# Performance work log

Hardware: AMD Instinct MI355X
Metric: run time of the kernel (lower is better)

## Reference

```python
import jax, jax.numpy as jnp
import numpy as np

B, S, I, H, C = 512, 128, 64, 256, 10


def setup_inputs() -> dict:
    key = jax.random.key(0)
    ks = jax.random.split(key, 9)
    u = lambda k, shape, lo, hi: jax.random.uniform(k, shape, jnp.float32, lo, hi)
    return {
        "x": jax.random.normal(ks[0], (B, S, I), jnp.float32),
        # LTCCell params (uniform init per init_parameters)
        "W_gd": u(ks[1], (2 * H, I + H), -0.1, 0.1),
        "b_gd": u(ks[2], (2 * H,), -0.1, 0.1),
        "W_tau": u(ks[3], (H, H), -0.1, 0.1),
        "b_tau": u(ks[4], (H,), -0.1, 0.1),
        "gleak": u(ks[5], (H,), 0.001, 1.0),
        "cm": u(ks[6], (H,), 0.4, 0.6),
        # classifier head
        "W_fc": jax.random.normal(ks[7], (C, H), jnp.float32) * 0.05,
        "b_fc": jax.random.normal(ks[8], (C,), jnp.float32) * 0.05,
    }


def reference(x, W_gd, b_gd, W_tau, b_tau, gleak, cm, W_fc, b_fc):
    # Constant part of the denominator (elementwise, hidden_dim)
    const_den = jax.nn.softplus(cm) + jax.nn.softplus(gleak)  # [H]

    def dhdt(h, x_t):
        # LTCCell.forward: dh/dt
        combined = jnp.concatenate([x_t, h], axis=1)          # [B, I+H]
        gd = combined @ W_gd.T + b_gd                          # [B, 2H]
        gate, dyn = jnp.split(gd, 2, axis=1)
        tau = jax.nn.softplus(h @ W_tau.T + b_tau)             # [B, H]
        num = jax.nn.sigmoid(gate) * jnp.tanh(dyn) - h
        return num / (tau + const_den + 1e-6)

    def step(h, x_t):
        # torchdiffeq 'rk4' fixed-grid = 3/8-rule RK4, single step dt=1 over [0,1]
        k1 = dhdt(h, x_t)
        k2 = dhdt(h + k1 / 3.0, x_t)
        k3 = dhdt(h + (k2 - k1 / 3.0), x_t)
        k4 = dhdt(h + (k1 - k2 + k3), x_t)
        h_new = h + (k1 + 3.0 * (k2 + k3) + k4) * 0.125
        return h_new, None

    h0 = jnp.zeros((x.shape[0], H), x.dtype)
    xs = jnp.transpose(x, (1, 0, 2))                           # [S, B, I]
    h_final, _ = jax.lax.scan(step, h0, xs)
    return h_final @ W_fc.T + b_fc                             # [B, C]
```

## Files before the change

### kernel.cpp

```cpp
#include <hip/hip_runtime.h>

typedef __attribute__((ext_vector_type(8))) short bf16x8;
typedef __attribute__((ext_vector_type(4))) float f32x4;
typedef __attribute__((ext_vector_type(2))) _Float16 f16x2;

#define MFMA(a, b, c) __builtin_amdgcn_mfma_f32_16x16x32_bf16((a), (b), (c), 0, 0, 0)

__device__ __forceinline__ unsigned short f2bf(float f) {
    unsigned int u = __builtin_bit_cast(unsigned int, f);
    return (unsigned short)((u + 0x7FFFu + ((u >> 16) & 1u)) >> 16);
}
__device__ __forceinline__ float softplusf(float v) {
    return __logf(1.f + __expf(v));
}

__global__ __launch_bounds__(256) void prepack_kernel(const float* __restrict__ W_gd,
                                                      unsigned short* __restrict__ ws) {
    int i = blockIdx.x * 256 + threadIdx.x;
    ws[i] = f2bf(W_gd[(256 + (i >> 8)) * 320 + 64 + (i & 255)]);
    if (i < 32768) ws[65536 + i] = f2bf(W_gd[(i >> 6) * 320 + (i & 63)]);
}

__global__ __launch_bounds__(512, 1)
void ltc_kernel(
    const float* __restrict__ x, const float* __restrict__ W_gd,
    const float* __restrict__ b_gd, const float* __restrict__ W_tau,
    const float* __restrict__ b_tau, const float* __restrict__ gleak,
    const float* __restrict__ cm, const float* __restrict__ W_fc,
    const float* __restrict__ b_fc, const unsigned short* __restrict__ ws,
    float* __restrict__ out)
{
    const int tid  = threadIdx.x;
    const int lane = tid & 63;
    const int wv   = tid >> 6;
    const int c16  = lane & 15;
    const int kg   = lane >> 4;
    const int kg8  = kg * 8;
    const int row0 = blockIdx.x * 2;

    __shared__ __align__(16) unsigned short tauL[65536];
    __shared__ __align__(16) unsigned short dynL[8192];
    __shared__ __align__(16) unsigned short abuf[2][264];
    __shared__ __align__(16) unsigned short xbuf[2][72];
    __shared__ __align__(8)  float tcL[512];
    __shared__ float bgdL[512];
    __shared__ float hout[2][257];

    for (int i = tid; i < 65536; i += 512) {
        int u = i >> 8, k = i & 255;
        tauL[u * 256 + (k ^ ((u & 15) << 3))] = f2bf(W_tau[i]);
    }
    for (int i = tid; i < 8192; i += 512) {
        int u = i >> 5, k = i & 31;
        dynL[u * 32 + (k ^ ((u & 3) << 3))] = f2bf(W_gd[(256 + u) * 320 + 64 + k]);
    }
    for (int i = tid; i < 2 * 264; i += 512) ((unsigned short*)abuf)[i] = 0;
    if (tid < 256) {
        tcL[2 * tid]     = b_tau[tid];
        tcL[2 * tid + 1] = softplusf(cm[tid]) + softplusf(gleak[tid]) + 1e-6f;
    }
    bgdL[tid] = b_gd[tid];

    const int uA = 32 * wv + c16;
    const int uB = uA + 16;
    const int tswz = c16 << 3;
    const unsigned short* tAb = tauL + uA * 256;
    const unsigned short* tBb = tauL + uB * 256;
    const bf16x8* dA0p = (const bf16x8*)(dynL + uA * 32 + (kg8 ^ ((c16 & 3) << 3)));
    const bf16x8* dB0p = (const bf16x8*)(dynL + uB * 32 + (kg8 ^ ((c16 & 3) << 3)));
    const unsigned short* sA  = ws + uA * 256 + kg8;
    const unsigned short* sB  = ws + uB * 256 + kg8;
    const unsigned short* wsx = ws + 65536;

    bf16x8 Wg[2][8];
    {
        const int wrow[2] = { uA, uB };
        #pragma unroll
        for (int t = 0; t < 2; ++t) {
            const float* src = W_gd + wrow[t] * 320 + 64;
            #pragma unroll
            for (int s = 0; s < 8; ++s) {
                const float4* p = (const float4*)(src + s * 32 + kg8);
                float4 a = p[0], b = p[1];
                bf16x8 v;
                v[0] = (short)f2bf(a.x); v[1] = (short)f2bf(a.y);
                v[2] = (short)f2bf(a.z); v[3] = (short)f2bf(a.w);
                v[4] = (short)f2bf(b.x); v[5] = (short)f2bf(b.y);
                v[6] = (short)f2bf(b.z); v[7] = (short)f2bf(b.w);
                Wg[t][s] = v;
            }
        }
    }

    const int rsel = (c16 < 2) ? c16 : 0;
    const unsigned short* aptr = &abuf[rsel][kg8];
    const unsigned short* xptr = &xbuf[rsel][kg8];

    float hv[2][2] = {{0.f, 0.f}, {0.f, 0.f}};
    f16x2 zh; zh[0] = (_Float16)0.f; zh[1] = (_Float16)0.f;
    f16x2 kk1[2] = { zh, zh }, kk2[2] = { zh, zh }, kk3[2] = { zh, zh };

    bf16x8 pipe[4];
    pipe[0] = *(const bf16x8*)(sA + 32);
    pipe[1] = *(const bf16x8*)(sA + 64);
    pipe[2] = *(const bf16x8*)(sA + 96);
    pipe[3] = *(const bf16x8*)(sA + 128);

    __syncthreads();

#define ELEM(ti, G, D, den, en)                                                  \
    _Pragma("unroll")                                                            \
    for (int r = 0; r < 2; ++r) {                                                \
        float gate = G[r] + (float)gdx[ti][r];                                   \
        float dyn  = D[r] + (float)gdx[2 + ti][r];                               \
        float sig = __fdividef(1.f, 1.f + __expf(-gate));                        \
        float th  = 1.f - __fdividef(2.f, __expf(2.f * dyn) + 1.f);              \
        float k1v = (float)kk1[ti][r], k2v = (float)kk2[ti][r], k3v = (float)kk3[ti][r]; \
        float h0 = hv[ti][r];                                                    \
        float ec;                                                                \
        if      (stg == 0) ec = h0;                                              \
        else if (stg == 1) ec = h0 + k1v * (1.f / 3.f);                          \
        else if (stg == 2) ec = h0 - k1v * (1.f / 3.f) + k2v;                    \
        else               ec = h0 + k1v - k2v + k3v;                            \
        float kv = __fdividef(sig * th - ec, den[r]);                            \
        if (stg == 0)      { kk1[ti][r] = (_Float16)kv; en[r] = h0 + kv * (1.f / 3.f); } \
        else if (stg == 1) { kk2[ti][r] = (_Float16)kv; en[r] = h0 - k1v * (1.f / 3.f) + kv; } \
        else if (stg == 2) { kk3[ti][r] = (_Float16)kv; en[r] = h0 + k1v - k2v + kv; } \
        else               { en[r] = h0 + 0.125f * (k1v + 3.f * (k2v + k3v) + kv); hv[ti][r] = en[r]; } \
    }

    #pragma unroll 1
    for (int ts = 0; ts < 128; ++ts) {
        if (tid < 128) {
            int r = tid >> 6, i = tid & 63;
            xbuf[r][i] = f2bf(x[((row0 + r) * 128 + ts) * 64 + i]);
        }
        __syncthreads();

        f32x4 gx0 = {0,0,0,0}, gx1 = {0,0,0,0}, gx2 = {0,0,0,0}, gx3 = {0,0,0,0};
        #pragma unroll
        for (int s = 0; s < 2; ++s) {
            bf16x8 ax = *(const bf16x8*)(xptr + s * 32);
            gx0 = MFMA(ax, *(const bf16x8*)(wsx + uA * 64         + s * 32 + kg8), gx0);
            gx1 = MFMA(ax, *(const bf16x8*)(wsx + uB * 64         + s * 32 + kg8), gx1);
            gx2 = MFMA(ax, *(const bf16x8*)(wsx + (256 + uA) * 64 + s * 32 + kg8), gx2);
            gx3 = MFMA(ax, *(const bf16x8*)(wsx + (256 + uB) * 64 + s * 32 + kg8), gx3);
        }
        f16x2 gdx[4];
        {
            float bg0 = bgdL[uA], bg1 = bgdL[uB], bg2 = bgdL[256 + uA], bg3 = bgdL[256 + uB];
            gdx[0][0] = (_Float16)(gx0[0] + bg0); gdx[0][1] = (_Float16)(gx0[1] + bg0);
            gdx[1][0] = (_Float16)(gx1[0] + bg1); gdx[1][1] = (_Float16)(gx1[1] + bg1);
            gdx[2][0] = (_Float16)(gx2[0] + bg2); gdx[2][1] = (_Float16)(gx2[1] + bg2);
            gdx[3][0] = (_Float16)(gx3[0] + bg3); gdx[3][1] = (_Float16)(gx3[1] + bg3);
        }

        #pragma unroll
        for (int stg = 0; stg < 4; ++stg) {
            f32x4 T0 = {0,0,0,0}, G0 = {0,0,0,0}, D0 = {0,0,0,0};
            {
                bf16x8 A = *(const bf16x8*)(aptr);
                T0 = MFMA(A, *(const bf16x8*)(tAb + (kg8 ^ tswz)), T0);
                G0 = MFMA(A, Wg[0][0], G0);
                D0 = MFMA(A, *dA0p, D0);
            }
            #pragma unroll
            for (int s = 1; s < 8; ++s) {
                bf16x8 A = *(const bf16x8*)(aptr + s * 32);
                T0 = MFMA(A, *(const bf16x8*)(tAb + ((s * 32 + kg8) ^ tswz)), T0);
                G0 = MFMA(A, Wg[0][s], G0);
                D0 = MFMA(A, pipe[(2 * stg + s - 1) & 3], D0);
                if (s + 3 < 7) pipe[(2 * stg + s + 3) & 3] = *(const bf16x8*)(sA + (s + 4) * 32);
                else           pipe[(2 * stg + s + 3) & 3] = *(const bf16x8*)(sB + (s - 3) * 32);
            }
            float2 tc0 = *(const float2*)(tcL + 2 * uA);
            float den0[2];
            den0[0] = softplusf(T0[0] + tc0.x) + tc0.y;
            den0[1] = softplusf(T0[1] + tc0.x) + tc0.y;
            float en0[2];
            ELEM(0, G0, D0, den0, en0);

            f32x4 T1 = {0,0,0,0}, G1 = {0,0,0,0}, D1 = {0,0,0,0};
            {
                bf16x8 A = *(const bf16x8*)(aptr);
                T1 = MFMA(A, *(const bf16x8*)(tBb + (kg8 ^ tswz)), T1);
                G1 = MFMA(A, Wg[1][0], G1);
                D1 = MFMA(A, *dB0p, D1);
            }
            #pragma unroll
            for (int s = 1; s < 8; ++s) {
                bf16x8 A = *(const bf16x8*)(aptr + s * 32);
                T1 = MFMA(A, *(const bf16x8*)(tBb + ((s * 32 + kg8) ^ tswz)), T1);
                G1 = MFMA(A, Wg[1][s], G1);
                D1 = MFMA(A, pipe[(2 * stg + 6 + s) & 3], D1);
                if (s <= 3) {
                    pipe[(2 * stg + 10 + s) & 3] = *(const bf16x8*)(sB + (s + 4) * 32);
                } else {
                    pipe[(2 * (stg + 1) + s - 4) & 3] = *(const bf16x8*)(sA + (s - 3) * 32);
                }
            }
            float2 tc1 = *(const float2*)(tcL + 2 * uB);
            float den1[2];
            den1[0] = softplusf(T1[0] + tc1.x) + tc1.y;
            den1[1] = softplusf(T1[1] + tc1.x) + tc1.y;
            float en1[2];
            ELEM(1, G1, D1, den1, en1);

            __syncthreads();
            if (lane < 16) {
                abuf[0][uA] = f2bf(en0[0]); abuf[1][uA] = f2bf(en0[1]);
                abuf[0][uB] = f2bf(en1[0]); abuf[1][uB] = f2bf(en1[1]);
            }
            __syncthreads();
        }
    }
#undef ELEM

    if (lane < 16) {
        hout[0][uA] = hv[0][0]; hout[1][uA] = hv[0][1];
        hout[0][uB] = hv[1][0]; hout[1][uB] = hv[1][1];
    }
    __syncthreads();
    if (tid < 20) {
        int r = tid / 10, c = tid % 10;
        float acc = b_fc[c];
        for (int k = 0; k < 256; ++k) acc = fmaf(hout[r][k], W_fc[c * 256 + k], acc);
        out[(row0 + r) * 10 + c] = acc;
    }
}

extern "C" void kernel_launch(void* const* d_in, const int* in_sizes, int n_in,
                              void* d_out, int out_size, void* d_ws, size_t ws_size,
                              hipStream_t stream) {
    (void)in_sizes; (void)n_in; (void)out_size; (void)ws_size;
    unsigned short* ws16 = (unsigned short*)d_ws;
    prepack_kernel<<<256, 256, 0, stream>>>((const float*)d_in[1], ws16);
    ltc_kernel<<<256, 512, 0, stream>>>(
        (const float*)d_in[0], (const float*)d_in[1], (const float*)d_in[2],
        (const float*)d_in[3], (const float*)d_in[4], (const float*)d_in[5],
        (const float*)d_in[6], (const float*)d_in[7], (const float*)d_in[8],
        ws16, (float*)d_out);
}
```

Before: 1.019 ms.

## Double-buffer hidden-state LDS to drop one barrier per RK stage

The bf16 hidden-state staging buffer is split into two ping-pong halves, so each RK stage reads one and writes the other. That removes the pre-write __syncthreads, and each half-tile's result is written right after it is computed. The dyn-weight prefetch ring is widened to five registers and restructured so the second tile streams all its dyn weights from global. The first tile's first chunk stays in a halved LDS table. The exchange is one fewer barrier per stage, at the cost of slightly more global/L2 weight traffic and more live registers.

```diff
diff --git a/kernel.cpp b/kernel.cpp
--- a/kernel.cpp
+++ b/kernel.cpp
@@ -39,8 +39,8 @@
     const int row0 = blockIdx.x * 2;
 
     __shared__ __align__(16) unsigned short tauL[65536];
-    __shared__ __align__(16) unsigned short dynL[8192];
-    __shared__ __align__(16) unsigned short abuf[2][264];
+    __shared__ __align__(16) unsigned short dynL[4096];
+    __shared__ __align__(16) unsigned short abuf[2][2][264];
     __shared__ __align__(16) unsigned short xbuf[2][72];
     __shared__ __align__(8)  float tcL[512];
     __shared__ float bgdL[512];
@@ -50,11 +50,12 @@
         int u = i >> 8, k = i & 255;
         tauL[u * 256 + (k ^ ((u & 15) << 3))] = f2bf(W_tau[i]);
     }
-    for (int i = tid; i < 8192; i += 512) {
-        int u = i >> 5, k = i & 31;
-        dynL[u * 32 + (k ^ ((u & 3) << 3))] = f2bf(W_gd[(256 + u) * 320 + 64 + k]);
-    }
-    for (int i = tid; i < 2 * 264; i += 512) ((unsigned short*)abuf)[i] = 0;
+    for (int i = tid; i < 4096; i += 512) {
+        int uidx = i >> 5, k = i & 31;
+        int u = (uidx >> 4) * 32 + (uidx & 15);
+        dynL[uidx * 32 + (k ^ ((uidx & 3) << 3))] = f2bf(W_gd[(256 + u) * 320 + 64 + k]);
+    }
+    for (int i = tid; i < 2 * 2 * 264; i += 512) ((unsigned short*)abuf)[i] = 0;
     if (tid < 256) {
         tcL[2 * tid]     = b_tau[tid];
         tcL[2 * tid + 1] = softplusf(cm[tid]) + softplusf(gleak[tid]) + 1e-6f;
@@ -66,11 +67,10 @@
     const int tswz = c16 << 3;
     const unsigned short* tAb = tauL + uA * 256;
     const unsigned short* tBb = tauL + uB * 256;
-    const bf16x8* dA0p = (const bf16x8*)(dynL + uA * 32 + (kg8 ^ ((c16 & 3) << 3)));
-    const bf16x8* dB0p = (const bf16x8*)(dynL + uB * 32 + (kg8 ^ ((c16 & 3) << 3)));
-    const unsigned short* sA  = ws + uA * 256 + kg8;
-    const unsigned short* sB  = ws + uB * 256 + kg8;
-    const unsigned short* wsx = ws + 65536;
+    const bf16x8* dA0p = (const bf16x8*)(dynL + (wv * 16 + c16) * 32 + (kg8 ^ ((c16 & 3) << 3)));
+    const int vOffA = uA * 256 + kg8;
+    const int vOffB = vOffA + 16 * 256;
+    const int vOffX = 65536 + uA * 64 + kg8;
 
     bf16x8 Wg[2][8];
     {
@@ -93,18 +93,18 @@
     }
 
     const int rsel = (c16 < 2) ? c16 : 0;
-    const unsigned short* aptr = &abuf[rsel][kg8];
-    const unsigned short* xptr = &xbuf[rsel][kg8];
+    const unsigned short* aptrP0 = &abuf[0][rsel][kg8];
+    const unsigned short* aptrP1 = &abuf[1][rsel][kg8];
+    const unsigned short* xptr   = &xbuf[rsel][kg8];
 
     float hv[2][2] = {{0.f, 0.f}, {0.f, 0.f}};
     f16x2 zh; zh[0] = (_Float16)0.f; zh[1] = (_Float16)0.f;
     f16x2 kk1[2] = { zh, zh }, kk2[2] = { zh, zh }, kk3[2] = { zh, zh };
 
-    bf16x8 pipe[4];
-    pipe[0] = *(const bf16x8*)(sA + 32);
-    pipe[1] = *(const bf16x8*)(sA + 64);
-    pipe[2] = *(const bf16x8*)(sA + 96);
-    pipe[3] = *(const bf16x8*)(sA + 128);
+    bf16x8 pipe[5];
+    #pragma unroll
+    for (int i = 0; i < 5; ++i)
+        pipe[i] = *(const bf16x8*)(ws + vOffA + (i + 1) * 32);
 
     __syncthreads();
 
@@ -141,10 +141,10 @@
         #pragma unroll
         for (int s = 0; s < 2; ++s) {
             bf16x8 ax = *(const bf16x8*)(xptr + s * 32);
-            gx0 = MFMA(ax, *(const bf16x8*)(wsx + uA * 64         + s * 32 + kg8), gx0);
-            gx1 = MFMA(ax, *(const bf16x8*)(wsx + uB * 64         + s * 32 + kg8), gx1);
-            gx2 = MFMA(ax, *(const bf16x8*)(wsx + (256 + uA) * 64 + s * 32 + kg8), gx2);
-            gx3 = MFMA(ax, *(const bf16x8*)(wsx + (256 + uB) * 64 + s * 32 + kg8), gx3);
+            gx0 = MFMA(ax, *(const bf16x8*)(ws + vOffX + s * 32), gx0);
+            gx1 = MFMA(ax, *(const bf16x8*)(ws + vOffX + 16 * 64 + s * 32), gx1);
+            gx2 = MFMA(ax, *(const bf16x8*)(ws + vOffX + 256 * 64 + s * 32), gx2);
+            gx3 = MFMA(ax, *(const bf16x8*)(ws + vOffX + 272 * 64 + s * 32), gx3);
         }
         f16x2 gdx[4];
         {
@@ -157,6 +157,9 @@
 
         #pragma unroll
         for (int stg = 0; stg < 4; ++stg) {
+            const unsigned short* aptr = (stg & 1) ? aptrP1 : aptrP0;
+            unsigned short (*wbuf)[264] = abuf[(stg & 1) ^ 1];
+
             f32x4 T0 = {0,0,0,0}, G0 = {0,0,0,0}, D0 = {0,0,0,0};
             {
                 bf16x8 A = *(const bf16x8*)(aptr);
@@ -169,9 +172,9 @@
                 bf16x8 A = *(const bf16x8*)(aptr + s * 32);
                 T0 = MFMA(A, *(const bf16x8*)(tAb + ((s * 32 + kg8) ^ tswz)), T0);
                 G0 = MFMA(A, Wg[0][s], G0);
-                D0 = MFMA(A, pipe[(2 * stg + s - 1) & 3], D0);
-                if (s + 3 < 7) pipe[(2 * stg + s + 3) & 3] = *(const bf16x8*)(sA + (s + 4) * 32);
-                else           pipe[(2 * stg + s + 3) & 3] = *(const bf16x8*)(sB + (s - 3) * 32);
+                D0 = MFMA(A, pipe[(s - 1) % 5], D0);
+                if (s <= 2) pipe[(s - 1) % 5] = *(const bf16x8*)(ws + vOffA + (s + 5) * 32);
+                else        pipe[(s - 1) % 5] = *(const bf16x8*)(ws + vOffB + (s - 3) * 32);
             }
             float2 tc0 = *(const float2*)(tcL + 2 * uA);
             float den0[2];
@@ -179,25 +182,17 @@
             den0[1] = softplusf(T0[1] + tc0.x) + tc0.y;
             float en0[2];
             ELEM(0, G0, D0, den0, en0);
+            if (lane < 16) { wbuf[0][uA] = f2bf(en0[0]); wbuf[1][uA] = f2bf(en0[1]); }
 
             f32x4 T1 = {0,0,0,0}, G1 = {0,0,0,0}, D1 = {0,0,0,0};
-            {
-                bf16x8 A = *(const bf16x8*)(aptr);
-                T1 = MFMA(A, *(const bf16x8*)(tBb + (kg8 ^ tswz)), T1);
-                G1 = MFMA(A, Wg[1][0], G1);
-                D1 = MFMA(A, *dB0p, D1);
-            }
             #pragma unroll
-            for (int s = 1; s < 8; ++s) {
+            for (int s = 0; s < 8; ++s) {
                 bf16x8 A = *(const bf16x8*)(aptr + s * 32);
                 T1 = MFMA(A, *(const bf16x8*)(tBb + ((s * 32 + kg8) ^ tswz)), T1);
                 G1 = MFMA(A, Wg[1][s], G1);
-                D1 = MFMA(A, pipe[(2 * stg + 6 + s) & 3], D1);
-                if (s <= 3) {
-                    pipe[(2 * stg + 10 + s) & 3] = *(const bf16x8*)(sB + (s + 4) * 32);
-                } else {
-                    pipe[(2 * (stg + 1) + s - 4) & 3] = *(const bf16x8*)(sA + (s - 3) * 32);
-                }
+                D1 = MFMA(A, pipe[(7 + s) % 5], D1);
+                if (s <= 2) pipe[(7 + s) % 5] = *(const bf16x8*)(ws + vOffB + (5 + s) * 32);
+                else        pipe[(7 + s) % 5] = *(const bf16x8*)(ws + vOffA + (s - 2) * 32);
             }
             float2 tc1 = *(const float2*)(tcL + 2 * uB);
             float den1[2];
@@ -205,12 +200,8 @@
             den1[1] = softplusf(T1[1] + tc1.x) + tc1.y;
             float en1[2];
             ELEM(1, G1, D1, den1, en1);
-
-            __syncthreads();
-            if (lane < 16) {
-                abuf[0][uA] = f2bf(en0[0]); abuf[1][uA] = f2bf(en0[1]);
-                abuf[0][uB] = f2bf(en1[0]); abuf[1][uB] = f2bf(en1[1]);
-            }
+            if (lane < 16) { wbuf[0][uB] = f2bf(en1[0]); wbuf[1][uB] = f2bf(en1[1]); }
+
             __syncthreads();
         }
     }
```

Result: no change. 1.013 ms (-0.6%).
